# Optimization experiments

Measured on AMD Instinct MI355X. Metric: run time of the kernel, lower is better.

## Reference

```python
import jax, jax.numpy as jnp
import numpy as np

B, V, H, E, Q = 32768, 2048, 256, 16, 4  # batch, num_visible, hidden_dim, num_experts, num_qubits
ENERGY_SCALE = 3.0
T_INIT, T_FINAL, N_STEPS = 1.0, 0.1, 100
SEED = 1  # annealing_counter after one call


def setup_inputs() -> dict:
    key = jax.random.key(0)
    ks = jax.random.split(key, 6)
    x = jax.random.normal(ks[0], (B, V), jnp.float32)
    We = jax.random.normal(ks[1], (V, H), jnp.float32) / np.sqrt(V).astype(np.float32)
    be = jnp.zeros((H,), jnp.float32)
    W1 = jax.random.normal(ks[2], (H + E, Q), jnp.float32) / np.sqrt(H + E).astype(np.float32)
    b1 = jnp.zeros((Q,), jnp.float32)
    w2 = jax.random.normal(ks[3], (Q,), jnp.float32) / np.sqrt(Q).astype(np.float32)
    b2 = jnp.zeros((), jnp.float32)
    inv_temp = jnp.ones((), jnp.float32)  # initial_inverse_temp = 1.0
    return dict(x=x, We=We, be=be, W1=W1, b1=b1, w2=w2, b2=b2, inv_temp=inv_temp)


def _energies(x, We, be, W1, b1, w2, b2):
    # feature_encoder: Dense(H, tanh)
    enc = jnp.tanh(x @ We + be)                       # [B, H]
    # combined = concat([enc tiled over experts, one_hot(expert)], -1) -> energy MLP.
    # one_hot @ W1[H:] just selects rows, so split the matmul instead of tiling:
    W1e, W1i = W1[:H], W1[H:]                         # [H,Q], [E,Q]
    h = jnp.tanh(enc @ W1e[None] if False else jnp.tanh((enc @ W1e)[:, None, :] + W1i[None, :, :] + b1))  # [B,E,Q]
    energies = ENERGY_SCALE * jnp.tanh(jnp.einsum('beq,q->be', h, w2) + b2)  # [B, E]
    return energies


def _qbm_sample(energies, seed):
    # Annealed Metropolis-Hastings over experts, geometric temperature schedule.
    key = jax.random.key(seed)
    kinit, kloop = jax.random.split(key)
    cur = jax.random.randint(kinit, (B,), 0, E)
    log_ratio = jnp.log(jnp.float32(T_FINAL / T_INIT))

    def step(cur, t):
        kt = jax.random.fold_in(kloop, t)
        kp, ku = jax.random.split(kt)
        frac = t.astype(jnp.float32) / jnp.float32(N_STEPS - 1)
        T = jnp.float32(T_INIT) * jnp.exp(log_ratio * frac)
        prop = jax.random.randint(kp, (B,), 0, E)
        e_prop = jnp.take_along_axis(energies, prop[:, None], 1)[:, 0]
        e_cur = jnp.take_along_axis(energies, cur[:, None], 1)[:, 0]
        accept = jax.random.uniform(ku, (B,)) < jnp.exp(jnp.minimum((e_cur - e_prop) / T, 0.0) + 0.0) * jnp.exp(jnp.minimum(-(e_prop - e_cur) / T, 0.0) * 0.0)
        # standard MH: accept if u < exp(-dE/T) (auto-accepts dE<=0)
        accept = jax.random.uniform(jax.random.fold_in(ku, 1), (B,)) < jnp.exp(jnp.minimum(-(e_prop - e_cur) / T, 0.0))
        return jnp.where(accept, prop, cur), None

    cur, _ = jax.lax.scan(step, cur, jnp.arange(N_STEPS))
    logp = jax.nn.log_softmax(-energies / jnp.float32(T_FINAL), axis=-1)
    sample_log_probs = jnp.take_along_axis(logp, cur[:, None], 1)[:, 0]
    final_e = jnp.take_along_axis(energies, cur[:, None], 1)[:, 0]
    return cur, sample_log_probs, final_e


def reference(x, We, be, W1, b1, w2, b2, inv_temp):
    energies = _energies(x, We, be, W1, b1, w2, b2)   # [B, E]
    beta = jax.nn.softplus(inv_temp)
    logits = -beta * energies
    # training=True, use_annealing=True path: stochastic expert selection
    assignments, _slp, _ae = _qbm_sample(jax.lax.stop_gradient(energies), SEED)
    probabilities = jax.nn.one_hot(assignments, E, dtype=jnp.float32)
    return probabilities, energies, logits
```

## Files before the change

### kernel.cpp

```cpp
#include <hip/hip_runtime.h>
#include <math.h>
#include <stdint.h>

#define B_N 32768
#define V_N 2048
#define H_N 256
#define E_N 16
#define Q_N 4

#define BROWS 32
#define KG_N (V_N/8)
#define NSS (V_N/128)

#define RNG_PART 1

typedef double f64x4 __attribute__((ext_vector_type(4)));
typedef float  f32x4 __attribute__((ext_vector_type(4)));
typedef short  bf16x8 __attribute__((ext_vector_type(8)));

union U8 { unsigned u[4]; bf16x8 v; };

#define TF_R(x0,x1,r) { x0 += x1; x1 = ((x1 << (r)) | (x1 >> (32-(r)))); x1 ^= x0; }

__device__ __forceinline__ void tf_block(uint32_t k0, uint32_t k1, uint32_t &x0, uint32_t &x1){
  uint32_t k2 = k0 ^ k1 ^ 0x1BD11BDAu;
  x0 += k0; x1 += k1;
  TF_R(x0,x1,13) TF_R(x0,x1,15) TF_R(x0,x1,26) TF_R(x0,x1,6)
  x0 += k1; x1 += k2 + 1u;
  TF_R(x0,x1,17) TF_R(x0,x1,29) TF_R(x0,x1,16) TF_R(x0,x1,24)
  x0 += k2; x1 += k0 + 2u;
  TF_R(x0,x1,13) TF_R(x0,x1,15) TF_R(x0,x1,26) TF_R(x0,x1,6)
  x0 += k0; x1 += k1 + 3u;
  TF_R(x0,x1,17) TF_R(x0,x1,29) TF_R(x0,x1,16) TF_R(x0,x1,24)
  x0 += k1; x1 += k2 + 4u;
  TF_R(x0,x1,13) TF_R(x0,x1,15) TF_R(x0,x1,26) TF_R(x0,x1,6)
  x0 += k2; x1 += k0 + 5u;
}

__device__ __forceinline__ int run_kats(){
  uint32_t x0, x1;
  x0 = 0u; x1 = 0u;
  tf_block(0u, 0u, x0, x1);
  if (x0 != 0x6b200159u || x1 != 0x99ba4efeu) return 1;
  x0 = 0xFFFFFFFFu; x1 = 0xFFFFFFFFu;
  tf_block(0xFFFFFFFFu, 0xFFFFFFFFu, x0, x1);
  if (x0 != 0x1cb996fcu || x1 != 0xbb002be7u) return 2;
  x0 = 0x243f6a88u; x1 = 0x85a308d3u;
  tf_block(0x13198a2eu, 0x03707344u, x0, x1);
  if (x0 != 0xc4923a9cu || x1 != 0x483df7a0u) return 3;
  return 0;
}

__device__ __forceinline__ uint32_t rbits(uint32_t ka, uint32_t kb, uint32_t b){
#if RNG_PART
  uint32_t x0 = 0u, x1 = b;
  tf_block(ka, kb, x0, x1);
  return x0 ^ x1;
#else
  uint32_t i = b & 16383u;
  uint32_t x0 = i, x1 = i + 16384u;
  tf_block(ka, kb, x0, x1);
  return (b < 16384u) ? x0 : x1;
#endif
}

__device__ __forceinline__ double exp_pos_f64(double v){
  const double LOG2E  = 1.4426950408889634074;
  const double LN2HI  = 6.93147180369123816490e-01;
  const double LN2LO  = 1.90821492927058770002e-10;
  double k = rint(v * LOG2E);
  double r = fma(-k, LN2HI, v);
  r = fma(-k, LN2LO, r);
  double p = 1.6059043836821613e-10;
  p = fma(p, r, 2.08767569878681e-09);
  p = fma(p, r, 2.505210838544172e-08);
  p = fma(p, r, 2.7557319223985893e-07);
  p = fma(p, r, 2.755731922398589e-06);
  p = fma(p, r, 2.48015873015873e-05);
  p = fma(p, r, 1.984126984126984e-04);
  p = fma(p, r, 1.3888888888888889e-03);
  p = fma(p, r, 8.333333333333333e-03);
  p = fma(p, r, 4.1666666666666664e-02);
  p = fma(p, r, 1.6666666666666666e-01);
  p = fma(p, r, 5.0e-01);
  p = fma(p, r, 1.0);
  p = fma(p, r, 1.0);
  int n = (int)k;
  double sc = __longlong_as_double(((long long)(1023 + n)) << 52);
  return p * sc;
}

__device__ __forceinline__ double tanh_fast(double x){
  double ax = fabs(x);
  if (ax < 0.25){
    double z = x * x;
    double p = 9.691537956929451e-05;
    p = fma(p, z, -2.3912911424355248e-04);
    p = fma(p, z,  5.900274409455859e-04);
    p = fma(p, z, -1.4558343870513183e-03);
    p = fma(p, z,  3.592128036572481e-03);
    p = fma(p, z, -8.863235529902197e-03);
    p = fma(p, z,  2.1869488536155203e-02);
    p = fma(p, z, -5.396825396825397e-02);
    p = fma(p, z,  1.3333333333333333e-01);
    p = fma(p, z, -3.3333333333333333e-01);
    double q = fma(p, z, 1.0);
    return x * q;
  }
  if (ax > 19.0) return copysign(1.0, x);
  double y = exp_pos_f64(2.0 * ax);
  double t = 1.0 - 2.0/(y + 1.0);
  return copysign(t, x);
}

__device__ __forceinline__ double tanh_d(double x, unsigned slow){
  return slow ? tanh(x) : tanh_fast(x);
}

__device__ __forceinline__ unsigned cvt_pk_bf16(float a, float b){
  unsigned r;
  asm("v_cvt_pk_bf16_f32 %0, %1, %2" : "=v"(r) : "v"(a), "v"(b));
  return r;
}

template<bool CV>
__device__ __forceinline__ void splitpair(float a, float b, unsigned &uh, unsigned &um, unsigned &ul){
  float ha, hb, ma, mb;
  if (CV){
    uh = cvt_pk_bf16(a, b);
    ha = __uint_as_float(uh<<16); hb = __uint_as_float(uh & 0xFFFF0000u);
  } else {
    unsigned ua=__float_as_uint(a), ub=__float_as_uint(b);
    uh = (ua>>16) | (ub & 0xFFFF0000u);
    ha = __uint_as_float(ua & 0xFFFF0000u); hb = __uint_as_float(ub & 0xFFFF0000u);
  }
  float ra = a - ha, rb = b - hb;
  if (CV){
    um = cvt_pk_bf16(ra, rb);
    ma = __uint_as_float(um<<16); mb = __uint_as_float(um & 0xFFFF0000u);
  } else {
    unsigned va=__float_as_uint(ra), vb=__float_as_uint(rb);
    um = (va>>16) | (vb & 0xFFFF0000u);
    ma = __uint_as_float(va & 0xFFFF0000u); mb = __uint_as_float(vb & 0xFFFF0000u);
  }
  float sa = ra - ma, sb = rb - mb;
  if (CV) ul = cvt_pk_bf16(sa, sb);
  else    ul = (__float_as_uint(sa)>>16) | (__float_as_uint(sb) & 0xFFFF0000u);
}

template<bool CV>
__device__ __forceinline__ void split8(const float* v, bf16x8& fh, bf16x8& fm, bf16x8& fl){
  U8 H, M, L;
  #pragma unroll
  for (int p=0;p<4;++p)
    splitpair<CV>(v[2*p], v[2*p+1], H.u[p], M.u[p], L.u[p]);
  fh=H.v; fm=M.v; fl=L.v;
}

__device__ __forceinline__ float bslot(bf16x8 f, int j){
  return __uint_as_float(((unsigned)(unsigned short)f[j]) << 16);
}

__device__ __forceinline__ float gate_val(unsigned idx){
  unsigned mant = (idx * 2654435761u) & 0x7FFFFFu;
  unsigned ex = 127u + (idx*7u)%8u - 4u;
  unsigned sgn = (idx & 1u) << 31;
  return __uint_as_float(sgn | (ex<<23) | mant);
}

__device__ __forceinline__ double Aref(int i, int k){ return 0.5 + 0.03*i - 0.7*k + 0.011*i*k; }
__device__ __forceinline__ double Bref(int k, int j){ return 1.1*k - 0.17*j + 0.019*j*k + 0.23; }
__device__ __forceinline__ int Aint(int i, int k){ return ((i*5 + k*3) % 13) - 6; }
__device__ __forceinline__ int Bint(int k, int j){ return ((k*7 + j*11) % 17) - 8; }

__global__ __launch_bounds__(1024) void init_kernel(unsigned* __restrict__ wsu, float log_ratio,
    const float* __restrict__ invt, const float* __restrict__ We,
    bf16x8* __restrict__ Bh, bf16x8* __restrict__ Bm, bf16x8* __restrict__ Bl, int presplit){
#pragma clang fp contract(off)
  __shared__ int sbad, sbadc, sbadt;
  int t = threadIdx.x;
  if (t == 0){ sbad = 0; sbadc = 0; sbadt = 0; }
  __syncthreads();

  if (blockIdx.x != 0){
    if (!presplit) return;
    {
      float xv[8];
      #pragma unroll
      for (int p=0;p<8;++p) xv[p] = gate_val((unsigned)(t*8+p));
      bf16x8 h,m,l;
      int badc=0, badt=0;
      split8<true>(xv,h,m,l);
      #pragma unroll
      for (int p=0;p<8;++p){
        double s = (double)bslot(h,p)+(double)bslot(m,p)+(double)bslot(l,p);
        if (s != (double)xv[p]) badc=1;
        if (fabsf(bslot(m,p)) > fabsf(xv[p])*0.00784f) badc=1;
      }
      split8<false>(xv,h,m,l);
      #pragma unroll
      for (int p=0;p<8;++p){
        double s = (double)bslot(h,p)+(double)bslot(m,p)+(double)bslot(l,p);
        if (s != (double)xv[p]) badt=1;
      }
      if (badc) atomicOr(&sbadc, 1);
      if (badt) atomicOr(&sbadt, 1);
    }
    __syncthreads();
    unsigned spl = sbadc ? (sbadt ? 2u : 1u) : 0u;
    if (spl >= 2u) return;
    int kg = (blockIdx.x - 1)*4 + (t >> 8);
    int col = t & 255;
    float v[8];
    #pragma unroll
    for (int i=0;i<8;++i)
      v[i] = We[(size_t)(kg*8+i)*H_N + col];
    bf16x8 h, m, l;
    if (spl == 0u) split8<true >(v, h, m, l);
    else           split8<false>(v, h, m, l);
    size_t o = (size_t)kg*H_N + col;
    Bh[o] = h; Bm[o] = m; Bl[o] = l;
    return;
  }

  {
    int bad = 0;
    for (int i = 0; i < 64; ++i){
      int idx = t * 64 + i;
      double x = -20.0 + 40.0 * ((double)idx + 0.5) / 65536.0;
      double a = tanh_fast(x);
      double b = tanh(x);
      if ((float)a != (float)b) bad = 1;
      long long ia = __double_as_longlong(a), ib = __double_as_longlong(b);
      long long d = ia - ib; if (d < 0) d = -d;
      if (d > 8) bad = 1;
    }
    if (bad) atomicOr(&sbad, 1);
  }

  {
    float xv[8];
    #pragma unroll
    for (int p=0;p<8;++p) xv[p] = gate_val((unsigned)(t*8+p));
    bf16x8 h,m,l;
    int badc=0, badt=0;
    split8<true>(xv,h,m,l);
    #pragma unroll
    for (int p=0;p<8;++p){
      double s = (double)bslot(h,p)+(double)bslot(m,p)+(double)bslot(l,p);
      if (s != (double)xv[p]) badc=1;
      if (fabsf(bslot(m,p)) > fabsf(xv[p])*0.00784f) badc=1;
    }
    split8<false>(xv,h,m,l);
    #pragma unroll
    for (int p=0;p<8;++p){
      double s = (double)bslot(h,p)+(double)bslot(m,p)+(double)bslot(l,p);
      if (s != (double)xv[p]) badt=1;
    }
    if (badc) atomicOr(&sbadc, 1);
    if (badt) atomicOr(&sbadt, 1);
  }

  if (t < 64){
    int l = t;
    int lr = l & 15, g = l >> 4;
    {
      double aval = Aref(lr, g);
      double bval = Bref(g, lr);
      int found = 8;
      for (int combo = 0; combo < 8; ++combo){
        int swap = combo & 1, drow = (combo>>1)&1, dt = (combo>>2)&1;
        f64x4 c = {0.0,0.0,0.0,0.0};
        if (swap) c = __builtin_amdgcn_mfma_f64_16x16x4f64(bval, aval, c, 0,0,0);
        else      c = __builtin_amdgcn_mfma_f64_16x16x4f64(aval, bval, c, 0,0,0);
        int bad = 0;
        #pragma unroll
        for (int r=0;r<4;++r){
          int f = drow ? (g + 4*r) : (4*g + r);
          int row = dt ? lr : f;
          int col = dt ? f  : lr;
          double e = 0.0;
          #pragma unroll
          for (int k=0;k<4;++k) e += Aref(row,k)*Bref(k,col);
          if (fabs(c[r] - e) > 1e-9) bad = 1;
        }
        if (__ballot(bad != 0) == 0ull){ found = combo; break; }
      }
      if (l == 0) wsu[503] = (unsigned)found;
    }
    {
      bf16x8 af, bf;
      #pragma unroll
      for (int j=0;j<8;++j){
        af[j] = (short)(__float_as_uint((float)Aint(lr, g*8+j)) >> 16);
        bf[j] = (short)(__float_as_uint((float)Bint(g*8+j, lr)) >> 16);
      }
      int found = 8;
      for (int combo = 0; combo < 8; ++combo){
        int swap = combo & 1, drow = (combo>>1)&1, dt = (combo>>2)&1;
        f32x4 c = {0.f,0.f,0.f,0.f};
        if (swap) c = __builtin_amdgcn_mfma_f32_16x16x32_bf16(bf, af, c, 0,0,0);
        else      c = __builtin_amdgcn_mfma_f32_16x16x32_bf16(af, bf, c, 0,0,0);
        int bad = 0;
        #pragma unroll
        for (int r=0;r<4;++r){
          int f = drow ? (g + 4*r) : (4*g + r);
          int row = dt ? lr : f;
          int col = dt ? f  : lr;
          int e = 0;
          for (int k=0;k<32;++k) e += Aint(row,k)*Bint(k,col);
          if (c[r] != (float)e) bad = 1;
        }
        if (__ballot(bad != 0) == 0ull){ found = combo; break; }
      }
      if (l == 0) wsu[506] = (unsigned)found;
    }
  }
  __syncthreads();
  if (t == 0){
    wsu[504] = (unsigned)sbad;
    wsu[507] = sbadc ? (sbadt ? 2u : 1u) : 0u;
  }

  uint32_t ka = 0u, kb = 1u;
  uint32_t kinit0, kinit1, kl0, kl1;
#if RNG_PART
  { uint32_t a0=0u,a1=0u; tf_block(ka,kb,a0,a1); kinit0=a0; kinit1=a1; }
  { uint32_t a0=0u,a1=1u; tf_block(ka,kb,a0,a1); kl0=a0; kl1=a1; }
#else
  { uint32_t c00=0u,c01=2u; tf_block(ka,kb,c00,c01);
    uint32_t c10=1u,c11=3u; tf_block(ka,kb,c10,c11);
    kinit0=c00; kinit1=c10; kl0=c01; kl1=c11; }
#endif
  if (t == 0){
    wsu[502] = (unsigned)run_kats();
    wsu[505] = __float_as_uint(-(float)log1p(exp((double)invt[0])));
#if RNG_PART
    uint32_t x0=0u, x1=1u; tf_block(kinit0,kinit1,x0,x1);
    wsu[500]=x0; wsu[501]=x1;
#else
    uint32_t e00=0u,e01=2u; tf_block(kinit0,kinit1,e00,e01);
    uint32_t e10=1u,e11=3u; tf_block(kinit0,kinit1,e10,e11);
    wsu[500]=e01; wsu[501]=e11;
#endif
  }
  if (t < 100){
    uint32_t kt0=0u, kt1=(uint32_t)t; tf_block(kl0,kl1,kt0,kt1);
    uint32_t q0, q1, v0, v1;
#if RNG_PART
    uint32_t p0=0u,p1=0u; tf_block(kt0,kt1,p0,p1);
    uint32_t u0=0u,u1=1u; tf_block(kt0,kt1,u0,u1);
    { uint32_t a=0u,b=1u; tf_block(p0,p1,a,b); q0=a; q1=b; }
    { uint32_t a=0u,b=1u; tf_block(u0,u1,a,b); v0=a; v1=b; }
#else
    uint32_t d00=0u,d01=2u; tf_block(kt0,kt1,d00,d01);
    uint32_t d10=1u,d11=3u; tf_block(kt0,kt1,d10,d11);
    uint32_t kp0=d00, kp1=d10, ku0=d01, ku1k=d11;
    uint32_t e00=0u,e01=2u; tf_block(kp0,kp1,e00,e01);
    uint32_t e10=1u,e11=3u; tf_block(kp0,kp1,e10,e11);
    q0=e01; q1=e11;
    { uint32_t a=0u,b=1u; tf_block(ku0,ku1k,a,b); v0=a; v1=b; }
#endif
    float fr = (float)t / 99.0f;
    float arg = log_ratio * fr;
    float T = (float)exp((double)arg);
    wsu[t*5+0]=q0; wsu[t*5+1]=q1; wsu[t*5+2]=v0; wsu[t*5+3]=v1;
    wsu[t*5+4]=__float_as_uint(T);
  }
}

template<bool SWAP, bool CV>
__device__ __forceinline__ void bf16_gemm_lds(
    const float* __restrict__ x,
    const bf16x8* __restrict__ Bh, const bf16x8* __restrict__ Bm, const bf16x8* __restrict__ Bl,
    bf16x8* Ahs, bf16x8* Ams, bf16x8* Als,
    f32x4 c8[2][2], double hh64[2][2][4],
    int tid, int wave, int lr, int lk, int row0)
{
  f32x4 hh[2][2];
  #pragma unroll
  for (int rt=0;rt<2;++rt)
    #pragma unroll
    for (int j=0;j<2;++j){
      hh[rt][j] = (f32x4){0.f,0.f,0.f,0.f};
      c8[rt][j] = (f32x4){0.f,0.f,0.f,0.f};
      #pragma unroll
      for (int r=0;r<4;++r) hh64[rt][j][r] = 0.0;
    }

#define MMB(a,b,c) (SWAP ? __builtin_amdgcn_mfma_f32_16x16x32_bf16((b),(a),(c),0,0,0) \
                         : __builtin_amdgcn_mfma_f32_16x16x32_bf16((a),(b),(c),0,0,0))

  const int col0 = wave*32 + lr;
  const int col1 = col0 + 16;
  const int srow = tid >> 4;
  const int skg  = tid & 15;
  const float* xp = x + (size_t)(row0 + srow)*V_N + skg*8;

  for (int ss=0; ss<NSS; ++ss){
    {
      float v[8];
      *(float4*)(v)   = *(const float4*)(xp + ss*128);
      *(float4*)(v+4) = *(const float4*)(xp + ss*128 + 4);
      bf16x8 h, m, l;
      split8<CV>(v, h, m, l);
      Ahs[skg*33 + srow] = h;
      Ams[skg*33 + srow] = m;
      Als[skg*33 + srow] = l;
    }
    __syncthreads();

    #pragma unroll
    for (int half=0; half<2; ++half){
      #pragma unroll
      for (int kin2=0; kin2<2; ++kin2){
        const int kgl = (half*2 + kin2)*4 + lk;
        const int kg  = ss*16 + kgl;
        const size_t bbase = (size_t)kg*H_N;
        bf16x8 bh0 = Bh[bbase + col0];
        bf16x8 bm0 = Bm[bbase + col0];
        bf16x8 bl0 = Bl[bbase + col0];
        bf16x8 bh1 = Bh[bbase + col1];
        bf16x8 bm1 = Bm[bbase + col1];
        bf16x8 bl1 = Bl[bbase + col1];
        bf16x8 ah[2], am[2], al[2];
        ah[0] = Ahs[kgl*33 + lr];      am[0] = Ams[kgl*33 + lr];      al[0] = Als[kgl*33 + lr];
        ah[1] = Ahs[kgl*33 + 16 + lr]; am[1] = Ams[kgl*33 + 16 + lr]; al[1] = Als[kgl*33 + 16 + lr];
        #pragma unroll
        for (int rt=0;rt<2;++rt){
          hh[rt][0] = MMB(ah[rt], bh0, hh[rt][0]);
          c8[rt][0] = MMB(ah[rt], bm0, c8[rt][0]);
          c8[rt][0] = MMB(am[rt], bh0, c8[rt][0]);
          c8[rt][0] = MMB(ah[rt], bl0, c8[rt][0]);
          c8[rt][0] = MMB(am[rt], bm0, c8[rt][0]);
          c8[rt][0] = MMB(al[rt], bh0, c8[rt][0]);
          hh[rt][1] = MMB(ah[rt], bh1, hh[rt][1]);
          c8[rt][1] = MMB(ah[rt], bm1, c8[rt][1]);
          c8[rt][1] = MMB(am[rt], bh1, c8[rt][1]);
          c8[rt][1] = MMB(ah[rt], bl1, c8[rt][1]);
          c8[rt][1] = MMB(am[rt], bm1, c8[rt][1]);
          c8[rt][1] = MMB(al[rt], bh1, c8[rt][1]);
        }
      }
      #pragma unroll
      for (int rt=0;rt<2;++rt)
        #pragma unroll
        for (int j=0;j<2;++j){
          #pragma unroll
          for (int r=0;r<4;++r) hh64[rt][j][r] += (double)hh[rt][j][r];
          hh[rt][j] = (f32x4){0.f,0.f,0.f,0.f};
        }
    }
    __syncthreads();
  }
#undef MMB
}

template<bool SWAP, bool CV>
__device__ __forceinline__ void bf16_gemm(
    const float* __restrict__ x, const float* __restrict__ We,
    f32x4 c8[2][2], double hh64[2][2][4],
    int wave, int lr, int lk, int row0)
{
  f32x4 hh[2][2];
  #pragma unroll
  for (int rt=0;rt<2;++rt)
    #pragma unroll
    for (int j=0;j<2;++j){
      hh[rt][j] = (f32x4){0.f,0.f,0.f,0.f};
      c8[rt][j] = (f32x4){0.f,0.f,0.f,0.f};
      #pragma unroll
      for (int r=0;r<4;++r) hh64[rt][j][r] = 0.0;
    }

#define MMB(a,b,c) (SWAP ? __builtin_amdgcn_mfma_f32_16x16x32_bf16((b),(a),(c),0,0,0) \
                         : __builtin_amdgcn_mfma_f32_16x16x32_bf16((a),(b),(c),0,0,0))

  const float* xr0 = x + (size_t)(row0 + lr)*V_N + lk*8;
  const float* xr1 = x + (size_t)(row0 + 16 + lr)*V_N + lk*8;

  for (int s=0; s<32; ++s){
    #pragma unroll
    for (int kin=0;kin<2;++kin){
      float bv0[8], bv1[8];
      const float* bp = We + ((size_t)(s*64 + kin*32 + lk*8))*H_N + wave*32 + lr;
      #pragma unroll
      for (int jj=0;jj<8;++jj){ bv0[jj] = bp[(size_t)jj*H_N]; bv1[jj] = bp[(size_t)jj*H_N + 16]; }
      bf16x8 bh0,bm0,bl0,bh1,bm1,bl1;
      split8<CV>(bv0, bh0, bm0, bl0);
      split8<CV>(bv1, bh1, bm1, bl1);
      bf16x8 ah[2], am[2], al[2];
      float av[8];
      *(float4*)(av)   = *(const float4*)(xr0 + s*64 + kin*32);
      *(float4*)(av+4) = *(const float4*)(xr0 + s*64 + kin*32 + 4);
      split8<CV>(av, ah[0], am[0], al[0]);
      *(float4*)(av)   = *(const float4*)(xr1 + s*64 + kin*32);
      *(float4*)(av+4) = *(const float4*)(xr1 + s*64 + kin*32 + 4);
      split8<CV>(av, ah[1], am[1], al[1]);
      #pragma unroll
      for (int rt=0;rt<2;++rt){
        hh[rt][0] = MMB(ah[rt], bh0, hh[rt][0]);
        c8[rt][0] = MMB(ah[rt], bm0, c8[rt][0]);
        c8[rt][0] = MMB(am[rt], bh0, c8[rt][0]);
        c8[rt][0] = MMB(ah[rt], bl0, c8[rt][0]);
        c8[rt][0] = MMB(am[rt], bm0, c8[rt][0]);
        c8[rt][0] = MMB(al[rt], bh0, c8[rt][0]);
        hh[rt][1] = MMB(ah[rt], bh1, hh[rt][1]);
        c8[rt][1] = MMB(ah[rt], bm1, c8[rt][1]);
        c8[rt][1] = MMB(am[rt], bh1, c8[rt][1]);
        c8[rt][1] = MMB(ah[rt], bl1, c8[rt][1]);
        c8[rt][1] = MMB(am[rt], bm1, c8[rt][1]);
        c8[rt][1] = MMB(al[rt], bh1, c8[rt][1]);
      }
    }
    #pragma unroll
    for (int rt=0;rt<2;++rt)
      #pragma unroll
      for (int j=0;j<2;++j){
        #pragma unroll
        for (int r=0;r<4;++r) hh64[rt][j][r] += (double)hh[rt][j][r];
        hh[rt][j] = (f32x4){0.f,0.f,0.f,0.f};
      }
  }
#undef MMB
}

__device__ __forceinline__ void valu_gemm_and_enc(
    const float* __restrict__ x, const float* __restrict__ We, const float* __restrict__ be,
    float* enc_s, int tid, int row0, unsigned slowtanh)
{
  const int rg = tid >> 6;
  const int c0 = (tid & 63) * 4;
  double acc[4][4];
  #pragma unroll
  for (int r=0;r<4;++r){ acc[r][0]=0.0; acc[r][1]=0.0; acc[r][2]=0.0; acc[r][3]=0.0; }

  for (int v=0; v<V_N; ++v){
    const float* wp = We + (size_t)v*H_N + c0;
    double w0=(double)wp[0], w1=(double)wp[1], w2d=(double)wp[2], w3=(double)wp[3];
    #pragma unroll
    for (int r4=0;r4<4;++r4){
      double xv = (double)x[(size_t)(row0+rg*4+r4)*V_N + v];
      acc[r4][0] = fma(xv, w0, acc[r4][0]);
      acc[r4][1] = fma(xv, w1, acc[r4][1]);
      acc[r4][2] = fma(xv, w2d, acc[r4][2]);
      acc[r4][3] = fma(xv, w3, acc[r4][3]);
    }
  }
  #pragma unroll
  for (int r4=0;r4<4;++r4){
    int r = rg*4 + r4;
    #pragma unroll
    for (int j=0;j<4;++j){
      int c = c0 + j;
      float m1 = (float)(acc[r4][j] + (double)be[c]);
      enc_s[r*257 + c] = (float)tanh_d((double)m1, slowtanh);
    }
  }
}

__global__ __launch_bounds__(512) void ke_kernel(
    const float* __restrict__ x, const float* __restrict__ We,
    const float* __restrict__ be, const float* __restrict__ W1,
    const float* __restrict__ b1, const float* __restrict__ w2,
    const float* __restrict__ b2, const float* __restrict__ invt,
    const unsigned* __restrict__ wsu,
    const bf16x8* __restrict__ Bh, const bf16x8* __restrict__ Bm,
    const bf16x8* __restrict__ Bl, int presplit,
    float* __restrict__ energ, float* __restrict__ logit,
    float* __restrict__ probs){
#pragma clang fp contract(off)
  __shared__ float smemf[BROWS*257];
  __shared__ double t2p[BROWS*4*4];
  __shared__ float t2_s[BROWS*4];
  float* enc_s = smemf;
  bf16x8* Ahs = (bf16x8*)smemf;
  bf16x8* Ams = Ahs + 16*33;
  bf16x8* Als = Ams + 16*33;
  float* en_s = smemf;
  float* us   = smemf + 512;
  unsigned* ps = (unsigned*)(smemf + 3712);

  const int tid = threadIdx.x;
  const int wave = tid >> 6;
  const int l = tid & 63;
  const int lr = l & 15;
  const int lk = l >> 4;
  const int row0 = blockIdx.x * BROWS;

  const unsigned combo16 = wsu[506];
  const unsigned splmode = wsu[507];
  const unsigned slowtanh = wsu[504];
  const unsigned katflag = wsu[502];
  const float nbeta = __uint_as_float(wsu[505]);

  if (combo16 < 8u && splmode < 2u){
    f32x4 c8[2][2];
    double hh64[2][2][4];
    const bool sw = (combo16 & 1u);
    if (presplit){
      if (splmode == 0u){
        if (sw) bf16_gemm_lds<true ,true >(x, Bh, Bm, Bl, Ahs, Ams, Als, c8, hh64, tid, wave, lr, lk, row0);
        else    bf16_gemm_lds<false,true >(x, Bh, Bm, Bl, Ahs, Ams, Als, c8, hh64, tid, wave, lr, lk, row0);
      } else {
        if (sw) bf16_gemm_lds<true ,false>(x, Bh, Bm, Bl, Ahs, Ams, Als, c8, hh64, tid, wave, lr, lk, row0);
        else    bf16_gemm_lds<false,false>(x, Bh, Bm, Bl, Ahs, Ams, Als, c8, hh64, tid, wave, lr, lk, row0);
      }
    } else if (splmode == 0u){
      if (sw) bf16_gemm<true ,true >(x, We, c8, hh64, wave, lr, lk, row0);
      else    bf16_gemm<false,true >(x, We, c8, hh64, wave, lr, lk, row0);
    } else {
      if (sw) bf16_gemm<true ,false>(x, We, c8, hh64, wave, lr, lk, row0);
      else    bf16_gemm<false,false>(x, We, c8, hh64, wave, lr, lk, row0);
    }
    __syncthreads();
    const int drow = (combo16 >> 1) & 1, dt = (combo16 >> 2) & 1;
    #pragma unroll
    for (int rt=0;rt<2;++rt){
      #pragma unroll
      for (int j=0;j<2;++j){
        #pragma unroll
        for (int r=0;r<4;++r){
          int f = drow ? (lk + 4*r) : (4*lk + r);
          int m = dt ? lr : f;
          int n = dt ? f  : lr;
          int row = rt*16 + m;
          int col = wave*32 + j*16 + n;
          double tot = hh64[rt][j][r] + (double)c8[rt][j][r] + (double)be[col];
          float m1 = (float)tot;
          enc_s[row*257 + col] = (float)tanh_d((double)m1, slowtanh);
        }
      }
    }
  } else {
    valu_gemm_and_enc(x, We, be, enc_s, tid, row0, slowtanh);
  }
  __syncthreads();

  {
    int r = tid >> 4, q = (tid >> 2) & 3, seg = tid & 3;
    double s = 0.0;
    const float* er = enc_s + r*257 + seg*64;
    const float* wq = W1 + seg*64*4 + q;
    #pragma unroll 8
    for (int hh=0; hh<64; ++hh)
      s = fma((double)er[hh], (double)wq[hh*4], s);
    t2p[(r*4+q)*4 + seg] = s;
  }
  __syncthreads();
  if (tid < 128){
    double s = ((t2p[tid*4+0] + t2p[tid*4+1]) + t2p[tid*4+2]) + t2p[tid*4+3];
    t2_s[tid] = (float)s;
  }
  __syncthreads();

  {
    int r = tid >> 4, e = tid & 15;
    float y = 0.0f;
    #pragma unroll
    for (int q=0;q<4;++q){
      float a1f = t2_s[r*4+q] + W1[(H_N+e)*4+q];
      float a2f = a1f + b1[q];
      float hin  = (float)tanh_d((double)a2f, slowtanh);
      float hout = (float)tanh_d((double)hin, slowtanh);
      y = y + hout * w2[q];
    }
    float yb = y + b2[0];
    float en = 3.0f * (float)tanh_d((double)yb, slowtanh);
    size_t gi = (size_t)(row0 + r)*E_N + e;
    energ[gi] = en;
    logit[gi] = nbeta * en;
    en_s[r*16 + e] = en;
  }

  if (katflag == 0u){
    for (int i = tid; i < 3200; i += 512){
      int t = i >> 5;
      int row = i & 31;
      uint32_t b = (uint32_t)(row0 + row);
      uint32_t prop = rbits(wsu[t*5+0], wsu[t*5+1], b) & 15u;
      uint32_t ru   = rbits(wsu[t*5+2], wsu[t*5+3], b);
      us[t*32 + row] = __uint_as_float((ru >> 9) | 0x3f800000u) - 1.0f;
      ps[t*32 + row] = prop;
    }
  }
  __syncthreads();

  if (tid < 32){
    const int row = tid;
    float* op = probs + (size_t)(row0 + row)*E_N;
    if (katflag != 0u){
      float c = 0.10f + 0.05f * (float)katflag;
      #pragma unroll
      for (int j0=0; j0<16; j0+=4){
        float4 r4; r4.x=c; r4.y=c; r4.z=c; r4.w=c;
        *(float4*)(op + j0) = r4;
      }
    } else {
      const float* se = en_s + row*16;
      uint32_t cur = rbits(wsu[500], wsu[501], (uint32_t)(row0 + row)) & 15u;
      for (int t=0; t<100; ++t){
        float T = __uint_as_float(wsu[t*5+4]);
        uint32_t prop = ps[t*32 + row];
        float u = us[t*32 + row];
        float ec = se[(int)cur];
        float ep = se[(int)prop];
        float z = (-(ep - ec)) / T;
        z = fminf(z, 0.0f);
        float a = (float)exp((double)z);
        cur = (u < a) ? prop : cur;
      }
      #pragma unroll
      for (int j0=0; j0<16; j0+=4){
        float4 r4;
        r4.x = (cur == (uint32_t)(j0+0)) ? 1.0f : 0.0f;
        r4.y = (cur == (uint32_t)(j0+1)) ? 1.0f : 0.0f;
        r4.z = (cur == (uint32_t)(j0+2)) ? 1.0f : 0.0f;
        r4.w = (cur == (uint32_t)(j0+3)) ? 1.0f : 0.0f;
        *(float4*)(op + j0) = r4;
      }
    }
  }
}

extern "C" void kernel_launch(void* const* d_in, const int* in_sizes, int n_in,
                              void* d_out, int out_size, void* d_ws, size_t ws_size,
                              hipStream_t stream) {
  const float* x   = (const float*)d_in[0];
  const float* We  = (const float*)d_in[1];
  const float* be  = (const float*)d_in[2];
  const float* W1  = (const float*)d_in[3];
  const float* b1  = (const float*)d_in[4];
  const float* w2  = (const float*)d_in[5];
  const float* b2  = (const float*)d_in[6];
  const float* itp = (const float*)d_in[7];
  float* out = (float*)d_out;
  float* probs = out;
  float* energ = out + (size_t)B_N*E_N;
  float* logit = out + 2*(size_t)B_N*E_N;
  unsigned* wsu = (unsigned*)d_ws;

  const size_t bsz = (size_t)KG_N * H_N * 16;
  const size_t need = 4096 + 3*bsz;
  int presplit = (ws_size >= need) ? 1 : 0;
  char* base = (char*)d_ws + 4096;
  bf16x8* Bh = (bf16x8*)(base);
  bf16x8* Bm = (bf16x8*)(base + bsz);
  bf16x8* Bl = (bf16x8*)(base + 2*bsz);

  float log_ratio = (float)log((double)((float)0.1));

  hipLaunchKernelGGL(init_kernel, dim3(65), dim3(1024), 0, stream,
                     wsu, log_ratio, itp, We, Bh, Bm, Bl, presplit);
  hipLaunchKernelGGL(ke_kernel, dim3(B_N/BROWS), dim3(512), 0, stream,
                     x, We, be, W1, b1, w2, b2, itp, wsu,
                     Bh, Bm, Bl, presplit,
                     energ, logit, probs);
}
```

Measured before the change: 431.8 us.

## Double row tile to 64 with 2x8 wave grid and 1024-thread blocks

Raises rows per block from 32 to 64 and launches 1024 threads arranged as a 2x8 wave grid, so each presplit B-operand (We hi/mid/lo) tile loaded from global memory is reused across twice as many rows. The LDS A staging stride changes to 67 and the MH sampling buffers grow to match. The non-presplit MFMA path is removed and the VALU fallback is reorganised to one row per 16 threads. This halves block count and may lower occupancy through register pressure at 1024 threads.

New measurement: 459.7 us. 1.06x slower.

```diff
diff --git a/kernel.cpp b/kernel.cpp
--- a/kernel.cpp
+++ b/kernel.cpp
@@ -8,9 +8,10 @@
 #define E_N 16
 #define Q_N 4
 
-#define BROWS 32
+#define BROWS 64
 #define KG_N (V_N/8)
 #define NSS (V_N/128)
+#define ASTR 67
 
 #define RNG_PART 1
 
@@ -375,7 +376,7 @@
     const bf16x8* __restrict__ Bh, const bf16x8* __restrict__ Bm, const bf16x8* __restrict__ Bl,
     bf16x8* Ahs, bf16x8* Ams, bf16x8* Als,
     f32x4 c8[2][2], double hh64[2][2][4],
-    int tid, int wave, int lr, int lk, int row0)
+    int tid, int wr, int wc, int lr, int lk, int row0)
 {
   f32x4 hh[2][2];
   #pragma unroll
@@ -391,11 +392,13 @@
 #define MMB(a,b,c) (SWAP ? __builtin_amdgcn_mfma_f32_16x16x32_bf16((b),(a),(c),0,0,0) \
                          : __builtin_amdgcn_mfma_f32_16x16x32_bf16((a),(b),(c),0,0,0))
 
-  const int col0 = wave*32 + lr;
+  const int col0 = wc*32 + lr;
   const int col1 = col0 + 16;
+  const int arow = wr*32;
   const int srow = tid >> 4;
   const int skg  = tid & 15;
   const float* xp = x + (size_t)(row0 + srow)*V_N + skg*8;
+  const int sidx = skg*ASTR + srow;
 
   for (int ss=0; ss<NSS; ++ss){
     {
@@ -404,9 +407,9 @@
       *(float4*)(v+4) = *(const float4*)(xp + ss*128 + 4);
       bf16x8 h, m, l;
       split8<CV>(v, h, m, l);
-      Ahs[skg*33 + srow] = h;
-      Ams[skg*33 + srow] = m;
-      Als[skg*33 + srow] = l;
+      Ahs[sidx] = h;
+      Ams[sidx] = m;
+      Als[sidx] = l;
     }
     __syncthreads();
 
@@ -424,8 +427,8 @@
         bf16x8 bm1 = Bm[bbase + col1];
         bf16x8 bl1 = Bl[bbase + col1];
         bf16x8 ah[2], am[2], al[2];
-        ah[0] = Ahs[kgl*33 + lr];      am[0] = Ams[kgl*33 + lr];      al[0] = Als[kgl*33 + lr];
-        ah[1] = Ahs[kgl*33 + 16 + lr]; am[1] = Ams[kgl*33 + 16 + lr]; al[1] = Als[kgl*33 + 16 + lr];
+        ah[0] = Ahs[kgl*ASTR + arow + lr];      am[0] = Ams[kgl*ASTR + arow + lr];      al[0] = Als[kgl*ASTR + arow + lr];
+        ah[1] = Ahs[kgl*ASTR + arow + 16 + lr]; am[1] = Ams[kgl*ASTR + arow + 16 + lr]; al[1] = Als[kgl*ASTR + arow + 16 + lr];
         #pragma unroll
         for (int rt=0;rt<2;++rt){
           hh[rt][0] = MMB(ah[rt], bh0, hh[rt][0]);
@@ -456,110 +459,32 @@
 #undef MMB
 }
 
-template<bool SWAP, bool CV>
-__device__ __forceinline__ void bf16_gemm(
-    const float* __restrict__ x, const float* __restrict__ We,
-    f32x4 c8[2][2], double hh64[2][2][4],
-    int wave, int lr, int lk, int row0)
-{
-  f32x4 hh[2][2];
-  #pragma unroll
-  for (int rt=0;rt<2;++rt)
-    #pragma unroll
-    for (int j=0;j<2;++j){
-      hh[rt][j] = (f32x4){0.f,0.f,0.f,0.f};
-      c8[rt][j] = (f32x4){0.f,0.f,0.f,0.f};
-      #pragma unroll
-      for (int r=0;r<4;++r) hh64[rt][j][r] = 0.0;
-    }
-
-#define MMB(a,b,c) (SWAP ? __builtin_amdgcn_mfma_f32_16x16x32_bf16((b),(a),(c),0,0,0) \
-                         : __builtin_amdgcn_mfma_f32_16x16x32_bf16((a),(b),(c),0,0,0))
-
-  const float* xr0 = x + (size_t)(row0 + lr)*V_N + lk*8;
-  const float* xr1 = x + (size_t)(row0 + 16 + lr)*V_N + lk*8;
-
-  for (int s=0; s<32; ++s){
-    #pragma unroll
-    for (int kin=0;kin<2;++kin){
-      float bv0[8], bv1[8];
-      const float* bp = We + ((size_t)(s*64 + kin*32 + lk*8))*H_N + wave*32 + lr;
-      #pragma unroll
-      for (int jj=0;jj<8;++jj){ bv0[jj] = bp[(size_t)jj*H_N]; bv1[jj] = bp[(size_t)jj*H_N + 16]; }
-      bf16x8 bh0,bm0,bl0,bh1,bm1,bl1;
-      split8<CV>(bv0, bh0, bm0, bl0);
-      split8<CV>(bv1, bh1, bm1, bl1);
-      bf16x8 ah[2], am[2], al[2];
-      float av[8];
-      *(float4*)(av)   = *(const float4*)(xr0 + s*64 + kin*32);
-      *(float4*)(av+4) = *(const float4*)(xr0 + s*64 + kin*32 + 4);
-      split8<CV>(av, ah[0], am[0], al[0]);
-      *(float4*)(av)   = *(const float4*)(xr1 + s*64 + kin*32);
-      *(float4*)(av+4) = *(const float4*)(xr1 + s*64 + kin*32 + 4);
-      split8<CV>(av, ah[1], am[1], al[1]);
-      #pragma unroll
-      for (int rt=0;rt<2;++rt){
-        hh[rt][0] = MMB(ah[rt], bh0, hh[rt][0]);
-        c8[rt][0] = MMB(ah[rt], bm0, c8[rt][0]);
-        c8[rt][0] = MMB(am[rt], bh0, c8[rt][0]);
-        c8[rt][0] = MMB(ah[rt], bl0, c8[rt][0]);
-        c8[rt][0] = MMB(am[rt], bm0, c8[rt][0]);
-        c8[rt][0] = MMB(al[rt], bh0, c8[rt][0]);
-        hh[rt][1] = MMB(ah[rt], bh1, hh[rt][1]);
-        c8[rt][1] = MMB(ah[rt], bm1, c8[rt][1]);
-        c8[rt][1] = MMB(am[rt], bh1, c8[rt][1]);
-        c8[rt][1] = MMB(ah[rt], bl1, c8[rt][1]);
-        c8[rt][1] = MMB(am[rt], bm1, c8[rt][1]);
-        c8[rt][1] = MMB(al[rt], bh1, c8[rt][1]);
-      }
-    }
-    #pragma unroll
-    for (int rt=0;rt<2;++rt)
-      #pragma unroll
-      for (int j=0;j<2;++j){
-        #pragma unroll
-        for (int r=0;r<4;++r) hh64[rt][j][r] += (double)hh[rt][j][r];
-        hh[rt][j] = (f32x4){0.f,0.f,0.f,0.f};
-      }
-  }
-#undef MMB
-}
-
 __device__ __forceinline__ void valu_gemm_and_enc(
     const float* __restrict__ x, const float* __restrict__ We, const float* __restrict__ be,
     float* enc_s, int tid, int row0, unsigned slowtanh)
 {
-  const int rg = tid >> 6;
-  const int c0 = (tid & 63) * 4;
-  double acc[4][4];
+  const int r = tid >> 4;
+  const int c0 = (tid & 15) * 16;
+  double acc[16];
   #pragma unroll
-  for (int r=0;r<4;++r){ acc[r][0]=0.0; acc[r][1]=0.0; acc[r][2]=0.0; acc[r][3]=0.0; }
-
+  for (int j=0;j<16;++j) acc[j] = 0.0;
+
+  const float* xr = x + (size_t)(row0 + r)*V_N;
   for (int v=0; v<V_N; ++v){
+    double xv = (double)xr[v];
     const float* wp = We + (size_t)v*H_N + c0;
-    double w0=(double)wp[0], w1=(double)wp[1], w2d=(double)wp[2], w3=(double)wp[3];
-    #pragma unroll
-    for (int r4=0;r4<4;++r4){
-      double xv = (double)x[(size_t)(row0+rg*4+r4)*V_N + v];
-      acc[r4][0] = fma(xv, w0, acc[r4][0]);
-      acc[r4][1] = fma(xv, w1, acc[r4][1]);
-      acc[r4][2] = fma(xv, w2d, acc[r4][2]);
-      acc[r4][3] = fma(xv, w3, acc[r4][3]);
-    }
+    #pragma unroll
+    for (int j=0;j<16;++j)
+      acc[j] = fma(xv, (double)wp[j], acc[j]);
   }
   #pragma unroll
-  for (int r4=0;r4<4;++r4){
-    int r = rg*4 + r4;
-    #pragma unroll
-    for (int j=0;j<4;++j){
-      int c = c0 + j;
-      float m1 = (float)(acc[r4][j] + (double)be[c]);
-      enc_s[r*257 + c] = (float)tanh_d((double)m1, slowtanh);
-    }
-  }
-}
-
-__global__ __launch_bounds__(512) void ke_kernel(
+  for (int j=0;j<16;++j){
+    float m1 = (float)(acc[j] + (double)be[c0+j]);
+    enc_s[r*257 + c0 + j] = (float)tanh_d((double)m1, slowtanh);
+  }
+}
+
+__global__ __launch_bounds__(1024) void ke_kernel(
     const float* __restrict__ x, const float* __restrict__ We,
     const float* __restrict__ be, const float* __restrict__ W1,
     const float* __restrict__ b1, const float* __restrict__ w2,
@@ -575,14 +500,16 @@
   __shared__ float t2_s[BROWS*4];
   float* enc_s = smemf;
   bf16x8* Ahs = (bf16x8*)smemf;
-  bf16x8* Ams = Ahs + 16*33;
-  bf16x8* Als = Ams + 16*33;
+  bf16x8* Ams = Ahs + 16*ASTR;
+  bf16x8* Als = Ams + 16*ASTR;
   float* en_s = smemf;
-  float* us   = smemf + 512;
-  unsigned* ps = (unsigned*)(smemf + 3712);
+  float* us   = smemf + 1024;
+  unsigned* ps = (unsigned*)(smemf + 7424);
 
   const int tid = threadIdx.x;
   const int wave = tid >> 6;
+  const int wr = wave & 1;
+  const int wc = wave >> 1;
   const int l = tid & 63;
   const int lr = l & 15;
   const int lk = l >> 4;
@@ -594,24 +521,16 @@
   const unsigned katflag = wsu[502];
   const float nbeta = __uint_as_float(wsu[505]);
 
-  if (combo16 < 8u && splmode < 2u){
+  if (presplit && combo16 < 8u && splmode < 2u){
     f32x4 c8[2][2];
     double hh64[2][2][4];
     const bool sw = (combo16 & 1u);
-    if (presplit){
-      if (splmode == 0u){
-        if (sw) bf16_gemm_lds<true ,true >(x, Bh, Bm, Bl, Ahs, Ams, Als, c8, hh64, tid, wave, lr, lk, row0);
-        else    bf16_gemm_lds<false,true >(x, Bh, Bm, Bl, Ahs, Ams, Als, c8, hh64, tid, wave, lr, lk, row0);
-      } else {
-        if (sw) bf16_gemm_lds<true ,false>(x, Bh, Bm, Bl, Ahs, Ams, Als, c8, hh64, tid, wave, lr, lk, row0);
-        else    bf16_gemm_lds<false,false>(x, Bh, Bm, Bl, Ahs, Ams, Als, c8, hh64, tid, wave, lr, lk, row0);
-      }
-    } else if (splmode == 0u){
-      if (sw) bf16_gemm<true ,true >(x, We, c8, hh64, wave, lr, lk, row0);
-      else    bf16_gemm<false,true >(x, We, c8, hh64, wave, lr, lk, row0);
+    if (splmode == 0u){
+      if (sw) bf16_gemm_lds<true ,true >(x, Bh, Bm, Bl, Ahs, Ams, Als, c8, hh64, tid, wr, wc, lr, lk, row0);
+      else    bf16_gemm_lds<false,true >(x, Bh, Bm, Bl, Ahs, Ams, Als, c8, hh64, tid, wr, wc, lr, lk, row0);
     } else {
-      if (sw) bf16_gemm<true ,false>(x, We, c8, hh64, wave, lr, lk, row0);
-      else    bf16_gemm<false,false>(x, We, c8, hh64, wave, lr, lk, row0);
+      if (sw) bf16_gemm_lds<true ,false>(x, Bh, Bm, Bl, Ahs, Ams, Als, c8, hh64, tid, wr, wc, lr, lk, row0);
+      else    bf16_gemm_lds<false,false>(x, Bh, Bm, Bl, Ahs, Ams, Als, c8, hh64, tid, wr, wc, lr, lk, row0);
     }
     __syncthreads();
     const int drow = (combo16 >> 1) & 1, dt = (combo16 >> 2) & 1;
@@ -624,8 +543,8 @@
           int f = drow ? (lk + 4*r) : (4*lk + r);
           int m = dt ? lr : f;
           int n = dt ? f  : lr;
-          int row = rt*16 + m;
-          int col = wave*32 + j*16 + n;
+          int row = wr*32 + rt*16 + m;
+          int col = wc*32 + j*16 + n;
           double tot = hh64[rt][j][r] + (double)c8[rt][j][r] + (double)be[col];
           float m1 = (float)tot;
           enc_s[row*257 + col] = (float)tanh_d((double)m1, slowtanh);
@@ -648,7 +567,7 @@
     t2p[(r*4+q)*4 + seg] = s;
   }
   __syncthreads();
-  if (tid < 128){
+  if (tid < 256){
     double s = ((t2p[tid*4+0] + t2p[tid*4+1]) + t2p[tid*4+2]) + t2p[tid*4+3];
     t2_s[tid] = (float)s;
   }
@@ -674,19 +593,19 @@
   }
 
   if (katflag == 0u){
-    for (int i = tid; i < 3200; i += 512){
-      int t = i >> 5;
-      int row = i & 31;
+    for (int i = tid; i < 6400; i += 1024){
+      int t = i >> 6;
+      int row = i & 63;
       uint32_t b = (uint32_t)(row0 + row);
       uint32_t prop = rbits(wsu[t*5+0], wsu[t*5+1], b) & 15u;
       uint32_t ru   = rbits(wsu[t*5+2], wsu[t*5+3], b);
-      us[t*32 + row] = __uint_as_float((ru >> 9) | 0x3f800000u) - 1.0f;
-      ps[t*32 + row] = prop;
+      us[t*64 + row] = __uint_as_float((ru >> 9) | 0x3f800000u) - 1.0f;
+      ps[t*64 + row] = prop;
     }
   }
   __syncthreads();
 
-  if (tid < 32){
+  if (tid < 64){
     const int row = tid;
     float* op = probs + (size_t)(row0 + row)*E_N;
     if (katflag != 0u){
@@ -701,8 +620,8 @@
       uint32_t cur = rbits(wsu[500], wsu[501], (uint32_t)(row0 + row)) & 15u;
       for (int t=0; t<100; ++t){
         float T = __uint_as_float(wsu[t*5+4]);
-        uint32_t prop = ps[t*32 + row];
-        float u = us[t*32 + row];
+        uint32_t prop = ps[t*64 + row];
+        float u = us[t*64 + row];
         float ec = se[(int)cur];
         float ep = se[(int)prop];
         float z = (-(ep - ec)) / T;
@@ -752,7 +671,7 @@
 
   hipLaunchKernelGGL(init_kernel, dim3(65), dim3(1024), 0, stream,
                      wsu, log_ratio, itp, We, Bh, Bm, Bl, presplit);
-  hipLaunchKernelGGL(ke_kernel, dim3(B_N/BROWS), dim3(512), 0, stream,
+  hipLaunchKernelGGL(ke_kernel, dim3(B_N/BROWS), dim3(1024), 0, stream,
                      x, We, be, W1, b1, w2, b2, itp, wsu,
                      Bh, Bm, Bl, presplit,
                      energ, logit, probs);
```
